# Performance work log

Measured on AMD Instinct MI355X. Metric: run time of the kernel, lower is better.

Reference implementation:

```python
import jax, jax.numpy as jnp
import numpy as np

# eqx.nn.MLP(1, 6, hidden=64, depth=3) => Linear dims [1,64,64,64,6]
DIMS = [1, 64, 64, 64, 6]
LATENT = sum(DIMS[i] * DIMS[i + 1] + DIMS[i + 1] for i in range(len(DIMS) - 1))  # 8838
BATCH, TIME, DATA = 8, 256, 1


def setup_inputs() -> dict:
    key = jax.random.key(0)
    k1, k2, k3, k4, k5 = jax.random.split(key, 5)
    xs = jax.random.normal(k1, (BATCH, 1, TIME, DATA), jnp.float32)
    ts = jax.random.uniform(k2, (BATCH, TIME), dtype=jnp.float32)
    theta = 0.05 * jax.random.normal(k3, (LATENT,), jnp.float32)
    # near-identity A keeps the 256-step linear recurrence numerically stable
    A = jnp.eye(LATENT, dtype=jnp.float32) + 1e-4 * jax.random.normal(k4, (LATENT, LATENT), jnp.float32)
    B = 1e-2 * jax.random.normal(k5, (LATENT, DATA), jnp.float32)
    return {"xs": xs, "ts": ts, "theta": theta, "A": A, "B": B}


def _mlp_eval(theta_b, ts):
    # theta_b: (batch, LATENT) flattened per-batch MLP params (eqx order: W.ravel, b per layer)
    # ts: (batch, time) -> output (batch, time, 6)
    h = ts[..., None]  # (b, t, 1)
    bsz = theta_b.shape[0]
    o = 0
    n_layers = len(DIMS) - 1
    for i in range(n_layers):
        din, dout = DIMS[i], DIMS[i + 1]
        W = theta_b[:, o:o + din * dout].reshape(bsz, dout, din)
        o += din * dout
        b = theta_b[:, o:o + dout]
        o += dout
        h = jnp.einsum('bod,btd->bto', W, h) + b[:, None, :]
        if i < n_layers - 1:
            h = jax.nn.relu(h)
    return h


def reference(xs, ts, theta, A, B):
    # xs: (batch, K, time, data) -> scan over xs[:, 0] along time
    xs0 = jnp.swapaxes(xs[:, 0], 0, 1)  # (time, batch, data)
    theta0 = jnp.broadcast_to(theta, (xs.shape[0], LATENT))  # (batch, LATENT)

    def step(th, x):  # th: (batch, LATENT), x: (batch, data)
        return th @ A.T + x @ B.T, None

    th_final, _ = jax.lax.scan(step, theta0, xs0)
    return _mlp_eval(th_final, ts)  # (batch, time, 6)
```

## Files before the change

### kernel.cpp

```cpp
#include <hip/hip_runtime.h>

#define L_      8838
#define LP_     9216
#define MPOW    7
#define NSLOT   (MPOW + 1)
#define NFULL   2
#define CT      512
#define CWGRID  512
#define CWAVES  (CWGRID * (CT / 64))
#define TBLK    ((L_ + 7) / 8)
#define TDEPTH  12

#define BOFF 6.0e-4f
#define D16  (BOFF / 32768.0f)
#define DHI  (BOFF / 128.0f)
#define C2   (BOFF + 128.0f * D16)
#define QS   (32768.0f / BOFF)

typedef float        f32x4 __attribute__((ext_vector_type(4)));
typedef float        f32x2 __attribute__((ext_vector_type(2)));

__device__ __forceinline__ float ubf(unsigned int u, int b) {
    return (float)((u >> (8 * b)) & 255u);
}
__device__ __forceinline__ f32x2 lo2(f32x4 a) { return __builtin_shufflevector(a, a, 0, 1); }
__device__ __forceinline__ f32x2 hi2(f32x4 a) { return __builtin_shufflevector(a, a, 2, 3); }
__device__ __forceinline__ f32x2 mk2(float a, float b) { f32x2 t; t.x = a; t.y = b; return t; }

__device__ __forceinline__ f32x2 pk_fma3(f32x2 a, f32x2 b, f32x2 c) {
    f32x2 d;
    asm("v_pk_fma_f32 %0, %1, %2, %3" : "=v"(d) : "v"(a), "v"(b), "v"(c));
    return d;
}
__device__ __forceinline__ void pk_acc(f32x2& acc, f32x2 a, f32x2 b) {
    asm("v_pk_fma_f32 %0, %1, %2, %0" : "+v"(acc) : "v"(a), "v"(b));
}

__device__ __forceinline__ void stage_vec(const float* __restrict__ gin,
                                          const float* __restrict__ hin,
                                          float* sgf, float* shf)
{
    #pragma unroll
    for (int k = 0; k < LP_ / (2 * CT); ++k) {
        const int j2 = k * CT + (int)threadIdx.x;
        float g0 = 0.f, g1 = 0.f, h0 = 0.f, h1 = 0.f;
        if (2 * j2 < L_) {
            const f32x2 gp = *(const f32x2*)(gin + 2 * j2);
            const f32x2 hp = *(const f32x2*)(hin + 2 * j2);
            g0 = gp.x; g1 = gp.y; h0 = hp.x; h1 = hp.y;
        }
        *(f32x2*)(sgf + 2 * j2) = mk2(g0, g1);
        *(f32x2*)(shf + 2 * j2) = mk2(h0, h1);
    }
    __syncthreads();
}

__device__ __forceinline__ void red_store(float ag, float ah, int lane, int row,
                                          float* __restrict__ gout, float* __restrict__ hout)
{
    #pragma unroll
    for (int o = 32; o; o >>= 1) { ag += __shfl_xor(ag, o); ah += __shfl_xor(ah, o); }
    if (lane == 0) { gout[row] = ag; hout[row] = ah; }
}

template<bool LO, bool PF>
__device__ __forceinline__ void fma_row(const float* sgf, const float* shf, int lane,
                                        unsigned int (&mhA)[18], unsigned int (&mhB)[18],
                                        unsigned int (&mlA)[18], unsigned int (&mlB)[18],
                                        const unsigned char* RnH, const unsigned char* RnL,
                                        f32x2& accg, f32x2& acch)
{
    const f32x2 cS  = mk2(DHI, DHI);
    const f32x2 cO  = LO ? mk2(-C2, -C2) : mk2(-BOFF, -BOFF);
    const f32x2 cI  = mk2(0.00390625f, 0.00390625f);
    #pragma unroll
    for (int c = 0; c < 18; ++c) {
        const unsigned int hA = mhA[c], hB = mhB[c];
        unsigned int lA = 0, lB = 0;
        if constexpr (LO) { lA = mlA[c]; lB = mlB[c]; }
        if constexpr (PF) {
            mhA[c] = *(const unsigned int*)(RnH + c * 512);
            mhB[c] = *(const unsigned int*)(RnH + c * 512 + 256);
            if constexpr (LO) {
                mlA[c] = *(const unsigned int*)(RnL + c * 512);
                mlB[c] = *(const unsigned int*)(RnL + c * 512 + 256);
            }
        }
        const int jb = c * 512 + 4 * lane;
        const f32x4 vg0 = *(const f32x4*)(sgf + jb);
        const f32x4 vg1 = *(const f32x4*)(sgf + jb + 256);
        const f32x4 vh0 = *(const f32x4*)(shf + jb);
        const f32x4 vh1 = *(const f32x4*)(shf + jb + 256);

        f32x2 uA01 = mk2(ubf(hA, 0), ubf(hA, 1));
        f32x2 uA23 = mk2(ubf(hA, 2), ubf(hA, 3));
        f32x2 uB01 = mk2(ubf(hB, 0), ubf(hB, 1));
        f32x2 uB23 = mk2(ubf(hB, 2), ubf(hB, 3));
        if constexpr (LO) {
            uA01 = pk_fma3(mk2(ubf(lA, 0), ubf(lA, 1)), cI, uA01);
            uA23 = pk_fma3(mk2(ubf(lA, 2), ubf(lA, 3)), cI, uA23);
            uB01 = pk_fma3(mk2(ubf(lB, 0), ubf(lB, 1)), cI, uB01);
            uB23 = pk_fma3(mk2(ubf(lB, 2), ubf(lB, 3)), cI, uB23);
        }
        const f32x2 vA01 = pk_fma3(uA01, cS, cO);
        const f32x2 vA23 = pk_fma3(uA23, cS, cO);
        const f32x2 vB01 = pk_fma3(uB01, cS, cO);
        const f32x2 vB23 = pk_fma3(uB23, cS, cO);

        pk_acc(accg, vA01, lo2(vg0)); pk_acc(accg, vA23, hi2(vg0));
        pk_acc(accg, vB01, lo2(vg1)); pk_acc(accg, vB23, hi2(vg1));
        pk_acc(acch, vA01, lo2(vh0)); pk_acc(acch, vA23, hi2(vh0));
        pk_acc(acch, vB01, lo2(vh1)); pk_acc(acch, vB23, hi2(vh1));
    }
}

template<bool LO>
__global__ __launch_bounds__(CT)
void chain_pass(const unsigned char* __restrict__ GHi, const unsigned char* __restrict__ GLo,
                const float* __restrict__ gin, const float* __restrict__ hin,
                float* __restrict__ gout, float* __restrict__ hout)
{
    __shared__ __align__(16) float sgf[LP_], shf[LP_];
    stage_vec(gin, hin, sgf, shf);
    const int lane = threadIdx.x & 63;
    int row = blockIdx.x * (CT / 64) + ((int)threadIdx.x >> 6);

    unsigned int mhA[18], mhB[18], mlA[18], mlB[18];
    if (row < L_) {
        const unsigned char* RH = GHi + (size_t)row * LP_;
        const unsigned char* RL = GLo + (size_t)row * LP_;
        #pragma unroll
        for (int c = 0; c < 18; ++c) {
            mhA[c] = *(const unsigned int*)(RH + c * 512 + 4 * lane);
            mhB[c] = *(const unsigned int*)(RH + c * 512 + 256 + 4 * lane);
            if constexpr (LO) {
                mlA[c] = *(const unsigned int*)(RL + c * 512 + 4 * lane);
                mlB[c] = *(const unsigned int*)(RL + c * 512 + 256 + 4 * lane);
            }
        }
    }
    while (row < L_) {
        const int nrow = row + CWAVES;
        const unsigned char* RnH = GHi + (size_t)nrow * LP_ + 4 * lane;
        const unsigned char* RnL = GLo + (size_t)nrow * LP_ + 4 * lane;
        f32x2 accg = mk2(0.f, 0.f), acch = mk2(0.f, 0.f);
        if (nrow < L_) fma_row<LO, true >(sgf, shf, lane, mhA, mhB, mlA, mlB, RnH, RnL, accg, acch);
        else           fma_row<LO, false>(sgf, shf, lane, mhA, mhB, mlA, mlB, RnH, RnL, accg, acch);
        red_store(accg.x + accg.y, acch.x + acch.y, lane, row, gout, hout);
        row = nrow;
    }
}

__device__ __forceinline__ void quant4(const float x[4], int j0, int rdiag,
                                       unsigned int& hw, unsigned int& lw)
{
    hw = 0; lw = 0;
    #pragma unroll
    for (int e = 0; e < 4; ++e) {
        const float g = x[e] - ((j0 + e == rdiag) ? 1.f : 0.f);
        int q = __float2int_rn(fmaf(g, QS, 32768.0f));
        q = min(max(q, 0), 65535);
        const int h = min((q + 128) >> 8, 255);
        const int l = min(q - (h << 8) + 128, 255);
        hw |= (unsigned)h << (8 * e);
        lw |= (unsigned)l << (8 * e);
    }
}

__global__ __launch_bounds__(CT)
void transcode_kernel(const float* __restrict__ A,
                      unsigned char* __restrict__ GHi, unsigned char* __restrict__ GLo,
                      const float* __restrict__ Bv, const float* __restrict__ th,
                      float* __restrict__ gv0, float* __restrict__ hv0)
{
    if (blockIdx.x == 0) {
        for (int j = threadIdx.x; j < L_; j += CT) { gv0[j] = Bv[j]; hv0[j] = th[j]; }
    }
    const int lane = threadIdx.x & 63;
    const int row = blockIdx.x * (CT / 64) + ((int)threadIdx.x >> 6);
    if (row >= L_) return;
    const float* __restrict__ Arow = A + (size_t)row * L_;
    unsigned char* __restrict__ WH = GHi + (size_t)row * LP_;
    unsigned char* __restrict__ WL = GLo + (size_t)row * LP_;

    f32x4 buf[TDEPTH];
    #pragma unroll
    for (int i = 0; i < TDEPTH; ++i)
        buf[i] = *(const f32x4*)(Arow + i * 256 + lane * 4);

    #pragma unroll
    for (int it = 0; it < 34; ++it) {
        const int j0 = it * 256 + lane * 4;
        const f32x4 x = buf[it % TDEPTH];
        if (it + TDEPTH < 34)
            buf[it % TDEPTH] = *(const f32x4*)(Arow + (it + TDEPTH) * 256 + lane * 4);
        float y[4] = {x.x, x.y, x.z, x.w};
        unsigned int hw, lw;
        quant4(y, j0, row, hw, lw);
        *(unsigned int*)(WH + j0) = hw;
        *(unsigned int*)(WL + j0) = lw;
    }
    {
        const int j0 = 34 * 256 + lane * 4;
        float x[4];
        #pragma unroll
        for (int e = 0; e < 4; ++e) x[e] = (j0 + e < L_) ? Arow[j0 + e] : 0.f;
        unsigned int hw, lw;
        quant4(x, j0, row, hw, lw);
        *(unsigned int*)(WH + j0) = hw;
        *(unsigned int*)(WL + j0) = lw;
    }
}

__global__ __launch_bounds__(CT)
void chain_fallback(const float* __restrict__ A,
                    const float* __restrict__ gin, const float* __restrict__ hin,
                    float* __restrict__ gout, float* __restrict__ hout)
{
    __shared__ __align__(16) float sgf[LP_], shf[LP_];
    stage_vec(gin, hin, sgf, shf);
    const int lane = threadIdx.x & 63;
    int row = blockIdx.x * (CT / 64) + ((int)threadIdx.x >> 6);
    while (row < L_) {
        const float* __restrict__ Arow = A + (size_t)row * L_;
        float ag = 0.f, ah = 0.f;
        for (int it = 0; it < 36; ++it) {
            const int j0 = it * 256 + lane * 4;
            float x[4];
            if (j0 + 3 < L_) {
                const f32x4 v = *(const f32x4*)(Arow + j0);
                x[0] = v.x; x[1] = v.y; x[2] = v.z; x[3] = v.w;
            } else {
                #pragma unroll
                for (int e = 0; e < 4; ++e) x[e] = (j0 + e < L_) ? Arow[j0 + e] : 0.f;
            }
            const f32x4 vg = *(const f32x4*)(sgf + j0);
            const f32x4 vh = *(const f32x4*)(shf + j0);
            ag = fmaf(x[0], vg.x, fmaf(x[1], vg.y, fmaf(x[2], vg.z, fmaf(x[3], vg.w, ag))));
            ah = fmaf(x[0], vh.x, fmaf(x[1], vh.y, fmaf(x[2], vh.z, fmaf(x[3], vh.w, ah))));
        }
        #pragma unroll
        for (int o = 32; o; o >>= 1) { ag += __shfl_xor(ag, o); ah += __shfl_xor(ah, o); }
        if (lane == 0) {
            gout[row] = ag - sgf[row];
            hout[row] = ah - shf[row];
        }
        row += CWAVES;
    }
}

__global__ void coeff_kernel(const float* __restrict__ xs,
                             double* __restrict__ s, double* __restrict__ c256)
{
    const int lane = threadIdx.x;
    const int t0 = lane * 4;
    float xl[8][4];
    #pragma unroll
    for (int b = 0; b < 8; ++b)
        #pragma unroll
        for (int i = 0; i < 4; ++i)
            xl[b][i] = xs[b * 256 + t0 + i];

    double c[4] = {1.0, 1.0, 1.0, 1.0};
    for (int m = 0; m <= MPOW; ++m) {
        #pragma unroll
        for (int b = 0; b < 8; ++b) {
            double part = c[0] * xl[b][0] + c[1] * xl[b][1]
                        + c[2] * xl[b][2] + c[3] * xl[b][3];
            for (int o = 32; o; o >>= 1) part += __shfl_xor(part, o);
            if (lane == 0) s[m * 8 + b] = part;
        }
        #pragma unroll
        for (int i = 0; i < 4; ++i) {
            double k = (double)(255 - (t0 + i));
            c[i] *= (k - m) / (double)(m + 1);
        }
    }
    if (lane == 0) {
        double c2 = 1.0;
        for (int m = 0; m <= MPOW; ++m) { c256[m] = c2; c2 = c2 * (256.0 - m) / (double)(m + 1); }
    }
}

__global__ __launch_bounds__(256)
void combine_kernel(const float* __restrict__ gv, const float* __restrict__ hv,
                    const double* __restrict__ s, const double* __restrict__ c256,
                    float* __restrict__ pfin)
{
    int i = blockIdx.x * 256 + threadIdx.x;
    if (i >= L_) return;
    double acc[8] = {0, 0, 0, 0, 0, 0, 0, 0};
    double hs = 0.0;
    for (int m = 0; m <= MPOW; ++m) {
        double g = (double)gv[(size_t)m * L_ + i];
        double h = (double)hv[(size_t)m * L_ + i];
        hs += c256[m] * h;
        #pragma unroll
        for (int b = 0; b < 8; ++b) acc[b] += s[m * 8 + b] * g;
    }
    #pragma unroll
    for (int b = 0; b < 8; ++b)
        pfin[(size_t)b * L_ + i] = (float)(acc[b] + hs);
}

__global__ __launch_bounds__(64)
void mlp_kernel(const float* __restrict__ pfin, const float* __restrict__ ts,
                float* __restrict__ out)
{
    const int b = blockIdx.x;
    const int t = blockIdx.y * 64 + threadIdx.x;
    const float* __restrict__ p = pfin + (size_t)b * L_;
    const float tv = ts[b * 256 + t];

    float h1[64], h2[64];
    #pragma unroll
    for (int o = 0; o < 64; ++o)
        h1[o] = fmaxf(fmaf(p[o], tv, p[64 + o]), 0.f);
    #pragma unroll
    for (int o = 0; o < 64; ++o) {
        float a0 = p[4224 + o], a1 = 0.f, a2 = 0.f, a3 = 0.f;
        #pragma unroll
        for (int d = 0; d < 64; d += 4) {
            a0 = fmaf(p[128 + o * 64 + d + 0], h1[d + 0], a0);
            a1 = fmaf(p[128 + o * 64 + d + 1], h1[d + 1], a1);
            a2 = fmaf(p[128 + o * 64 + d + 2], h1[d + 2], a2);
            a3 = fmaf(p[128 + o * 64 + d + 3], h1[d + 3], a3);
        }
        h2[o] = fmaxf((a0 + a1) + (a2 + a3), 0.f);
    }
    #pragma unroll
    for (int o = 0; o < 64; ++o) {
        float a0 = p[8384 + o], a1 = 0.f, a2 = 0.f, a3 = 0.f;
        #pragma unroll
        for (int d = 0; d < 64; d += 4) {
            a0 = fmaf(p[4288 + o * 64 + d + 0], h2[d + 0], a0);
            a1 = fmaf(p[4288 + o * 64 + d + 1], h2[d + 1], a1);
            a2 = fmaf(p[4288 + o * 64 + d + 2], h2[d + 2], a2);
            a3 = fmaf(p[4288 + o * 64 + d + 3], h2[d + 3], a3);
        }
        h1[o] = fmaxf((a0 + a1) + (a2 + a3), 0.f);
    }
    #pragma unroll
    for (int o = 0; o < 6; ++o) {
        float a0 = p[8832 + o], a1 = 0.f, a2 = 0.f, a3 = 0.f;
        #pragma unroll
        for (int d = 0; d < 64; d += 4) {
            a0 = fmaf(p[8448 + o * 64 + d + 0], h1[d + 0], a0);
            a1 = fmaf(p[8448 + o * 64 + d + 1], h1[d + 1], a1);
            a2 = fmaf(p[8448 + o * 64 + d + 2], h1[d + 2], a2);
            a3 = fmaf(p[8448 + o * 64 + d + 3], h1[d + 3], a3);
        }
        out[((size_t)(b * 256 + t)) * 6 + o] = (a0 + a1) + (a2 + a3);
    }
}

extern "C" void kernel_launch(void* const* d_in, const int* in_sizes, int n_in,
                              void* d_out, int out_size, void* d_ws, size_t ws_size,
                              hipStream_t stream)
{
    const float* xs    = (const float*)d_in[0];
    const float* ts    = (const float*)d_in[1];
    const float* theta = (const float*)d_in[2];
    const float* A     = (const float*)d_in[3];
    const float* B     = (const float*)d_in[4];
    float* out = (float*)d_out;

    const size_t GB1 = (size_t)L_ * LP_;
    const size_t VB  = (size_t)NSLOT * L_ * sizeof(float);
    const size_t SB  = (size_t)NSLOT * 8 * sizeof(double);
    const size_t CB  = 256;
    const size_t PB  = (size_t)8 * L_ * sizeof(float);
    const size_t SMALL = 2 * VB + SB + CB + PB;
    const size_t FULL  = 2 * GB1 + SMALL;

    if (ws_size < SMALL) return;
    const bool fat = (ws_size >= FULL);

    char* base = (char*)d_ws;
    unsigned char* GHi = (unsigned char*)base;
    unsigned char* GLo = (unsigned char*)(base + GB1);
    size_t off = fat ? 2 * GB1 : 0;
    float*  gv   = (float*)(base + off);  off += VB;
    float*  hv   = (float*)(base + off);  off += VB;
    double* s    = (double*)(base + off); off += SB;
    double* c256 = (double*)(base + off); off += CB;
    float*  pfin = (float*)(base + off);

    coeff_kernel<<<1, 64, 0, stream>>>(xs, s, c256);

    if (fat) {
        transcode_kernel<<<dim3(TBLK), dim3(CT), 0, stream>>>(
            A, GHi, GLo, B, theta, gv, hv);
        for (int p = 0; p < MPOW; ++p) {
            const float* gi = gv + (size_t)p * L_;
            const float* hi = hv + (size_t)p * L_;
            float* go = gv + (size_t)(p + 1) * L_;
            float* ho = hv + (size_t)(p + 1) * L_;
            if (p < NFULL)
                chain_pass<true ><<<dim3(CWGRID), dim3(CT), 0, stream>>>(GHi, GLo, gi, hi, go, ho);
            else
                chain_pass<false><<<dim3(CWGRID), dim3(CT), 0, stream>>>(GHi, GLo, gi, hi, go, ho);
        }
    } else {
        hipMemcpyAsync(gv, B,     L_ * sizeof(float), hipMemcpyDeviceToDevice, stream);
        hipMemcpyAsync(hv, theta, L_ * sizeof(float), hipMemcpyDeviceToDevice, stream);
        for (int p = 0; p < MPOW; ++p)
            chain_fallback<<<dim3(CWGRID), dim3(CT), 0, stream>>>(A,
                gv + (size_t)p * L_,       hv + (size_t)p * L_,
                gv + (size_t)(p + 1) * L_, hv + (size_t)(p + 1) * L_);
    }

    combine_kernel<<<(L_ + 255) / 256, 256, 0, stream>>>(gv, hv, s, c256, pfin);
    mlp_kernel<<<dim3(8, 4), 64, 0, stream>>>(pfin, ts, out);
}
```

Baseline: 379.5 us.

## Stage transcode A-row loads through LDS with double-buffered global_load_lds

Rewrites the A-matrix transcode kernel so each block handles 8 rows in 2048-column chunks. It loads them with direct global-to-LDS loads into a double buffer, replacing the per-wave register prefetch of 12 vector loads. The goal is to cut register pressure and improve load pipelining while keeping byte-wise writes coalesced. In exchange it adds a block-wide barrier per chunk and uses 4-byte-per-lane LDS loads, which may issue more load instructions than the previous 16-byte loads.

```diff
diff --git a/kernel.cpp b/kernel.cpp
--- a/kernel.cpp
+++ b/kernel.cpp
@@ -8,8 +8,10 @@
 #define CT      512
 #define CWGRID  512
 #define CWAVES  (CWGRID * (CT / 64))
-#define TBLK    ((L_ + 7) / 8)
-#define TDEPTH  12
+#define TROWS   8
+#define TBLK    ((L_ + TROWS - 1) / TROWS)
+#define TCH     2048
+#define NCH     5
 
 #define BOFF 6.0e-4f
 #define D16  (BOFF / 32768.0f)
@@ -34,6 +36,12 @@
 }
 __device__ __forceinline__ void pk_acc(f32x2& acc, f32x2 a, f32x2 b) {
     asm("v_pk_fma_f32 %0, %1, %2, %0" : "+v"(acc) : "v"(a), "v"(b));
+}
+
+__device__ __forceinline__ void gload_lds4(const float* g, float* l) {
+    __builtin_amdgcn_global_load_lds(
+        (const __attribute__((address_space(1))) void*)g,
+        (__attribute__((address_space(3))) void*)l, 4, 0, 0);
 }
 
 __device__ __forceinline__ void stage_vec(const float* __restrict__ gin,
@@ -167,48 +175,56 @@
     }
 }
 
+__device__ __forceinline__ void t_issue(const float* __restrict__ A, int r0, int it,
+                                        float* sbuf, int wv, int lane)
+{
+    const int row = r0 + it / NCH;
+    const int c0  = (it % NCH) * TCH;
+    const float* __restrict__ Arow = A + (size_t)row * L_;
+    #pragma unroll
+    for (int j = 0; j < 4; ++j) {
+        const int idx = wv * 256 + j * 64;
+        const int col = min(c0 + idx + lane, L_ - 1);
+        gload_lds4(Arow + col, sbuf + idx);
+    }
+}
+
 __global__ __launch_bounds__(CT)
 void transcode_kernel(const float* __restrict__ A,
                       unsigned char* __restrict__ GHi, unsigned char* __restrict__ GLo,
                       const float* __restrict__ Bv, const float* __restrict__ th,
                       float* __restrict__ gv0, float* __restrict__ hv0)
 {
+    __shared__ __align__(16) float sbuf[2][TCH];
     if (blockIdx.x == 0) {
         for (int j = threadIdx.x; j < L_; j += CT) { gv0[j] = Bv[j]; hv0[j] = th[j]; }
     }
-    const int lane = threadIdx.x & 63;
-    const int row = blockIdx.x * (CT / 64) + ((int)threadIdx.x >> 6);
-    if (row >= L_) return;
-    const float* __restrict__ Arow = A + (size_t)row * L_;
-    unsigned char* __restrict__ WH = GHi + (size_t)row * LP_;
-    unsigned char* __restrict__ WL = GLo + (size_t)row * LP_;
-
-    f32x4 buf[TDEPTH];
-    #pragma unroll
-    for (int i = 0; i < TDEPTH; ++i)
-        buf[i] = *(const f32x4*)(Arow + i * 256 + lane * 4);
-
-    #pragma unroll
-    for (int it = 0; it < 34; ++it) {
-        const int j0 = it * 256 + lane * 4;
-        const f32x4 x = buf[it % TDEPTH];
-        if (it + TDEPTH < 34)
-            buf[it % TDEPTH] = *(const f32x4*)(Arow + (it + TDEPTH) * 256 + lane * 4);
-        float y[4] = {x.x, x.y, x.z, x.w};
-        unsigned int hw, lw;
-        quant4(y, j0, row, hw, lw);
-        *(unsigned int*)(WH + j0) = hw;
-        *(unsigned int*)(WL + j0) = lw;
-    }
-    {
-        const int j0 = 34 * 256 + lane * 4;
-        float x[4];
-        #pragma unroll
-        for (int e = 0; e < 4; ++e) x[e] = (j0 + e < L_) ? Arow[j0 + e] : 0.f;
-        unsigned int hw, lw;
-        quant4(x, j0, row, hw, lw);
-        *(unsigned int*)(WH + j0) = hw;
-        *(unsigned int*)(WL + j0) = lw;
+    const int tid = (int)threadIdx.x;
+    const int wv = tid >> 6, lane = tid & 63;
+    const int r0 = blockIdx.x * TROWS;
+    const int nrows = min(TROWS, L_ - r0);
+    const int nit = nrows * NCH;
+
+    t_issue(A, r0, 0, sbuf[0], wv, lane);
+    __syncthreads();
+    for (int it = 0; it < nit; ++it) {
+        if (it + 1 < nit)
+            t_issue(A, r0, it + 1, sbuf[(it + 1) & 1], wv, lane);
+        const int row = r0 + it / NCH;
+        const int c0  = (it % NCH) * TCH;
+        const int j0  = c0 + 4 * tid;
+        if (j0 < LP_) {
+            const f32x4 x = *(const f32x4*)&sbuf[it & 1][4 * tid];
+            float y[4];
+            #pragma unroll
+            for (int e = 0; e < 4; ++e)
+                y[e] = (j0 + e < L_) ? ((e == 0) ? x.x : (e == 1) ? x.y : (e == 2) ? x.z : x.w) : 0.f;
+            unsigned int hw, lw;
+            quant4(y, j0, row, hw, lw);
+            *(unsigned int*)(GHi + (size_t)row * LP_ + j0) = hw;
+            *(unsigned int*)(GLo + (size_t)row * LP_ + j0) = lw;
+        }
+        __syncthreads();
     }
 }
 
```

New measurement: 394.0 us. 3.8% more time.
